# Kernel tuning notes

Hardware: AMD Instinct MI355X
Metric: run time of the kernel (lower is better)

The kernel has to match this reference:

```python
import jax, jax.numpy as jnp
import numpy as np

B, S, IN, OUT = 8, 2048, 4096, 4096
SPARSE_FRACTION = 0.9
ALPHA = 0.3


def setup_inputs() -> dict:
    key = jax.random.key(0)
    k1, k2, k3 = jax.random.split(key, 3)
    total = IN * OUT
    target_nz = int(total * (1.0 - SPARSE_FRACTION))          # nonzeros after rigl step
    num_drop = int(ALPHA * target_nz)                          # = mask.sum() - target_nz
    # kaiming_uniform_(a=sqrt(5)) -> bound = 1/sqrt(fan_in)
    bound = 1.0 / np.sqrt(IN)
    weight = jax.random.uniform(k1, (OUT, IN), minval=-bound, maxval=bound, dtype=jnp.float32)
    x = jax.random.normal(k2, (B, S, IN), dtype=jnp.float32)
    dense_grad = jax.random.normal(k3, (OUT, IN), dtype=jnp.float32) * 0.01
    # mask starts with target_nz + num_drop nonzeros so the drop/grow path runs
    rng = np.random.default_rng(0)
    idx = rng.permutation(total)[: target_nz + num_drop]
    m = np.zeros(total, dtype=bool)
    m[idx] = True
    mask = jnp.asarray(m.reshape(OUT, IN))
    return {"x": x, "weight": weight, "dense_grad": dense_grad, "mask": mask, "num_drop": num_drop}


def _rigl_mask(weight, dense_grad, mask, num_drop):
    # RigL sparse-to-sparse update: drop smallest-|w|, grow largest-|grad| among masked-out slots.
    flat = mask.reshape(-1)
    if num_drop > 0:  # num_drop is a static Python int
        wmag = jnp.abs(weight).reshape(-1)
        _, drop_idx = jax.lax.top_k(-wmag, num_drop)           # smallest magnitudes
        flat = flat.at[drop_idx].set(False)
        gmag = jnp.abs(dense_grad).reshape(-1)
        grow_scores = jnp.where(flat, -jnp.inf, gmag)          # only grow where mask == 0
        _, grow_idx = jax.lax.top_k(grow_scores, num_drop)
        flat = flat.at[grow_idx].set(True)
    return flat.reshape(mask.shape)


def reference(x, weight, dense_grad, mask, num_drop):
    new_mask = _rigl_mask(weight, dense_grad, mask, num_drop)
    masked_weight = weight * new_mask.astype(weight.dtype)     # [OUT, IN]
    # F.linear: y = x @ W^T
    return jnp.einsum('bsi,oi->bso', x, masked_weight)
```

## Files before the change

### kernel.cpp

```cpp
#include <hip/hip_runtime.h>
#include <hip/hip_bf16.h>

#define M_TOT 16384
#define N_TOT 4096
#define K_TOT 4096
#define NELEM 16777216

typedef __attribute__((ext_vector_type(8))) short bf16x8;
typedef __attribute__((ext_vector_type(4))) float f32x4;

#define AS1 __attribute__((address_space(1)))
#define AS3 __attribute__((address_space(3)))

struct SelState {
  unsigned long long prefix;
  unsigned long long thr;
  unsigned int k_rem;
  unsigned int done;
  unsigned int active;
};

struct Ctl {
  unsigned long long pcount;
  unsigned int mask_is_byte;
  unsigned int cand_n;
  SelState d;
  SelState g;
};

__device__ Ctl g_ctl;
__device__ unsigned int g_hist[4096];
__device__ unsigned int g_ticket[4];
__device__ unsigned char g_elig[NELEM];
__device__ unsigned short g_wb[NELEM];
__device__ unsigned short g_xb[(size_t)M_TOT * K_TOT];
__device__ unsigned long long g_cand[NELEM];

__device__ __forceinline__ unsigned short f2bf(float f) {
  unsigned int u = __float_as_uint(f);
  unsigned int r = (u + 0x7FFFu + ((u >> 16) & 1u)) >> 16;
  return (unsigned short)r;
}

__device__ __forceinline__ unsigned long long key_drop_bits(unsigned int fb, int i) {
  unsigned int b = fb & 0x7FFFFFFFu;
  return (((unsigned long long)b) << 24) | (unsigned int)i;
}
__device__ __forceinline__ unsigned long long key_grow_bits(unsigned int fb, int i) {
  unsigned int b = ~(fb & 0x7FFFFFFFu);
  return (((unsigned long long)b) << 24) | (unsigned int)i;
}

__global__ void ctl_reset() {
  int t = threadIdx.x;
  if (t == 0) { g_ctl.pcount = 0ull; g_ctl.cand_n = 0u; }
  if (t < 4) g_ticket[t] = 0u;
  for (int i = t; i < 4096; i += 256) g_hist[i] = 0;
}

__global__ void mask_popcnt(const unsigned int* mw) {
  const int NW = NELEM / 4;
  unsigned int s = 0;
  for (int i = blockIdx.x * blockDim.x + threadIdx.x; i < NW; i += gridDim.x * blockDim.x)
    s += __popc(mw[i]);
  for (int off = 32; off > 0; off >>= 1) s += __shfl_down(s, off, 64);
  if ((threadIdx.x & 63) == 0)
    atomicAdd((unsigned long long*)&g_ctl.pcount, (unsigned long long)s);
}

__global__ void sel_init(const int* ndp) {
  unsigned int k = (unsigned int)ndp[0];
  g_ctl.mask_is_byte = (g_ctl.pcount > 1200000ull) ? 1u : 0u;
  SelState s;
  s.prefix = 0ull; s.thr = 0ull; s.k_rem = k;
  s.done = (k == 0u) ? 1u : 0u;
  s.active = (k > 0u) ? 1u : 0u;
  g_ctl.d = s;
  g_ctl.g = s;
}

__device__ void do_select_impl(unsigned int* hist, SelState* stp, int shift, int nbits) {
  __shared__ unsigned int sc[256];
  __shared__ int tgt;
  const int nb = 1 << nbits;
  const int per = (nb + 255) / 256;
  const int t = threadIdx.x;
  unsigned int s = 0;
  for (int j = 0; j < per; ++j) {
    int b = t * per + j;
    if (b < nb) s += hist[b];
  }
  sc[t] = s;
  __syncthreads();
  for (int off = 1; off < 256; off <<= 1) {
    unsigned int v = (t >= off) ? sc[t - off] : 0u;
    __syncthreads();
    sc[t] += v;
    __syncthreads();
  }
  const unsigned int k = stp->k_rem;
  const unsigned int cum = sc[t];
  const unsigned int before = cum - s;
  if (before < k && k <= cum) tgt = t;
  __syncthreads();
  if (t == tgt) {
    unsigned int c = before;
    for (int j = 0; j < per; ++j) {
      int b = t * per + j;
      unsigned int h = (b < nb) ? hist[b] : 0u;
      if (c + h >= k) {
        unsigned long long np = (stp->prefix << nbits) | (unsigned long long)(unsigned int)b;
        stp->prefix = np;
        stp->k_rem = k - c;
        stp->thr = ((np + 1ull) << shift) - 1ull;
        if (k - c == h) stp->done = 1;
        break;
      }
      c += h;
    }
  }
  __syncthreads();
  for (int b = t; b < nb; b += 256) hist[b] = 0;
}

template <int SEL>
__global__ __launch_bounds__(256) void histsel_full(const float* __restrict__ src) {
  SelState* stp = SEL ? &g_ctl.g : &g_ctl.d;
  if (stp->done) return;
  __shared__ unsigned int lh[4096];
  for (int i = threadIdx.x; i < 4096; i += 256) lh[i] = 0;
  __syncthreads();
  const int N4 = NELEM / 4;
  for (int q = blockIdx.x * blockDim.x + threadIdx.x; q < N4; q += gridDim.x * blockDim.x) {
    float4 v = ((const float4*)src)[q];
    float fv[4] = {v.x, v.y, v.z, v.w};
    unsigned char ev[4] = {1, 1, 1, 1};
    if (SEL) {
      uchar4 e4 = ((const uchar4*)g_elig)[q];
      ev[0] = e4.x; ev[1] = e4.y; ev[2] = e4.z; ev[3] = e4.w;
    }
#pragma unroll
    for (int j = 0; j < 4; ++j) {
      if (SEL && !ev[j]) continue;
      int i = q * 4 + j;
      unsigned int fb = __float_as_uint(fv[j]);
      unsigned long long key = SEL ? key_grow_bits(fb, i) : key_drop_bits(fb, i);
      atomicAdd(&lh[(unsigned int)(key >> 44)], 1u);
    }
  }
  __syncthreads();
  for (int i = threadIdx.x; i < 4096; i += 256)
    if (lh[i]) atomicAdd(&g_hist[i], lh[i]);
  __threadfence();
  __shared__ unsigned int tk;
  if (threadIdx.x == 0) tk = atomicAdd(&g_ticket[SEL], 1u);
  __syncthreads();
  if (tk != (unsigned int)gridDim.x - 1) return;
  __threadfence();
  do_select_impl(g_hist, stp, 44, 12);
}

#define CCAP 4096
template <int SEL>
__global__ __launch_bounds__(256) void compact_pass(const float* __restrict__ src) {
  SelState& st = SEL ? g_ctl.g : g_ctl.d;
  if (st.done) return;
  __shared__ unsigned long long lk[CCAP];
  __shared__ unsigned int ln;
  __shared__ unsigned int gbase;
  if (threadIdx.x == 0) ln = 0;
  __syncthreads();
  const unsigned long long pref = st.prefix;
  const int N4 = NELEM / 4;
  for (int q = blockIdx.x * blockDim.x + threadIdx.x; q < N4; q += gridDim.x * blockDim.x) {
    float4 v = ((const float4*)src)[q];
    float fv[4] = {v.x, v.y, v.z, v.w};
    unsigned char ev[4] = {1, 1, 1, 1};
    if (SEL) {
      uchar4 e4 = ((const uchar4*)g_elig)[q];
      ev[0] = e4.x; ev[1] = e4.y; ev[2] = e4.z; ev[3] = e4.w;
    }
#pragma unroll
    for (int j = 0; j < 4; ++j) {
      if (SEL && !ev[j]) continue;
      int i = q * 4 + j;
      unsigned int fb = __float_as_uint(fv[j]);
      unsigned long long key = SEL ? key_grow_bits(fb, i) : key_drop_bits(fb, i);
      if ((key >> 44) == pref) {
        unsigned int slot = atomicAdd(&ln, 1u);
        if (slot < CCAP) {
          lk[slot] = key;
        } else {
          unsigned int gb = atomicAdd(&g_ctl.cand_n, 1u);
          g_cand[gb] = key;
        }
      }
    }
  }
  __syncthreads();
  unsigned int n = ln < CCAP ? ln : CCAP;
  if (threadIdx.x == 0) gbase = atomicAdd(&g_ctl.cand_n, n);
  __syncthreads();
  for (unsigned int i = threadIdx.x; i < n; i += blockDim.x)
    g_cand[gbase + i] = lk[i];
}

template <int SEL>
__global__ __launch_bounds__(256) void hist_cand(int shift, int nbits) {
  SelState& st = SEL ? g_ctl.g : g_ctl.d;
  if (st.done) return;
  __shared__ unsigned int lh[4096];
  const int nb = 1 << nbits;
  for (int i = threadIdx.x; i < nb; i += blockDim.x) lh[i] = 0;
  __syncthreads();
  const unsigned long long pref = st.prefix;
  const unsigned int n = g_ctl.cand_n;
  for (unsigned int i = blockIdx.x * blockDim.x + threadIdx.x; i < n; i += gridDim.x * blockDim.x) {
    unsigned long long key = g_cand[i];
    if ((key >> (shift + nbits)) == pref)
      atomicAdd(&lh[(unsigned int)(key >> shift) & (unsigned int)(nb - 1)], 1u);
  }
  __syncthreads();
  for (int i = threadIdx.x; i < nb; i += blockDim.x)
    if (lh[i]) atomicAdd(&g_hist[i], lh[i]);
}

template <int SEL>
__global__ void select_pass(int shift, int nbits) {
  SelState* stp = SEL ? &g_ctl.g : &g_ctl.d;
  if (stp->done) return;
  do_select_impl(g_hist, stp, shift, nbits);
}

__global__ __launch_bounds__(256) void build_elig(const float* __restrict__ w, const void* maskp) {
  if (blockIdx.x == 0 && threadIdx.x == 0) g_ctl.cand_n = 0u;
  int q = blockIdx.x * blockDim.x + threadIdx.x;
  if (q >= NELEM / 4) return;
  float4 wv = ((const float4*)w)[q];
  float fv[4] = {wv.x, wv.y, wv.z, wv.w};
  unsigned char m[4];
  if (g_ctl.mask_is_byte) {
    uchar4 m4 = ((const uchar4*)maskp)[q];
    m[0] = m4.x; m[1] = m4.y; m[2] = m4.z; m[3] = m4.w;
  } else {
    int4 m4 = ((const int4*)maskp)[q];
    m[0] = m4.x != 0; m[1] = m4.y != 0; m[2] = m4.z != 0; m[3] = m4.w != 0;
  }
  const bool act = g_ctl.d.active;
  const unsigned long long thr = g_ctl.d.thr;
  uchar4 e;
  unsigned char ev[4];
#pragma unroll
  for (int j = 0; j < 4; ++j) {
    int i = q * 4 + j;
    bool dropped = act && (key_drop_bits(__float_as_uint(fv[j]), i) <= thr);
    ev[j] = (!m[j] || dropped) ? 1 : 0;
  }
  e.x = ev[0]; e.y = ev[1]; e.z = ev[2]; e.w = ev[3];
  ((uchar4*)g_elig)[q] = e;
}

__global__ __launch_bounds__(256) void build_wb(const float* __restrict__ w, const float* __restrict__ gr) {
  int q = blockIdx.x * blockDim.x + threadIdx.x;
  if (q >= NELEM / 4) return;
  float4 wv = ((const float4*)w)[q];
  float4 gv = ((const float4*)gr)[q];
  float wf[4] = {wv.x, wv.y, wv.z, wv.w};
  float gf[4] = {gv.x, gv.y, gv.z, gv.w};
  uchar4 e4 = ((const uchar4*)g_elig)[q];
  unsigned char ev[4] = {e4.x, e4.y, e4.z, e4.w};
  const bool act = g_ctl.g.active;
  const unsigned long long thr = g_ctl.g.thr;
  ushort4 o;
  unsigned short ov[4];
#pragma unroll
  for (int j = 0; j < 4; ++j) {
    int i = q * 4 + j;
    bool keep;
    if (!ev[j]) keep = true;
    else keep = act && (key_grow_bits(__float_as_uint(gf[j]), i) <= thr);
    ov[j] = keep ? f2bf(wf[j]) : (unsigned short)0;
  }
  o.x = ov[0]; o.y = ov[1]; o.z = ov[2]; o.w = ov[3];
  ((ushort4*)g_wb)[q] = o;
}

__global__ __launch_bounds__(256) void convert_x(const float* __restrict__ x) {
  int i = blockIdx.x * blockDim.x + threadIdx.x;
  float4 v = ((const float4*)x)[i];
  ushort4 o;
  o.x = f2bf(v.x); o.y = f2bf(v.y); o.z = f2bf(v.z); o.w = f2bf(v.w);
  ((ushort4*)g_xb)[i] = o;
}

#define BM2 256
#define BN2 256
#define BK2 64
#define NT2 (K_TOT / BK2)
#define BUFB (256 * 128)

__global__ __launch_bounds__(512, 2) void gemm_kernel(float* __restrict__ out) {
  __shared__ __align__(16) char smem[131072];
  unsigned short* Asb = (unsigned short*)smem;
  unsigned short* Bsb = (unsigned short*)(smem + 65536);
  const int tid = threadIdx.x;
  const int lane = tid & 63;
  const int w = tid >> 6;
  const int wm = w >> 2, wn = w & 3;

  const int orig = blockIdx.x;
  const int swz = (orig & 7) * 128 + (orig >> 3);
  const int gm0 = (swz >> 4) * BM2;
  const int gn0 = (swz & 15) * BN2;

  f32x4 acc[8][4];
#pragma unroll
  for (int i = 0; i < 8; ++i)
#pragma unroll
    for (int j = 0; j < 4; ++j) acc[i][j] = (f32x4){0.f, 0.f, 0.f, 0.f};

  const int sr = (w << 3) + (lane >> 3);
  const int sc = 8 * ((lane & 7) ^ (lane >> 3));
  const unsigned short* Agp = g_xb + (size_t)(gm0 + sr) * K_TOT + sc;
  const unsigned short* Bgp = g_wb + (size_t)(gn0 + sr) * K_TOT + sc;
  const int lr = (w << 3);

#define STAGE_A(tile, half) do {                                             \
    const int bi_ = (tile) & 1; const int kb_ = ((tile) & (NT2 - 1)) * BK2;  \
    __builtin_amdgcn_global_load_lds(                                        \
        (const AS1 void*)(Agp + (size_t)((half) * 128) * K_TOT + kb_),       \
        (AS3 void*)(Asb + (size_t)bi_ * (BM2 * BK2) +                        \
                    ((half) * 128 + lr) * BK2), 16, 0, 0);                   \
    __builtin_amdgcn_global_load_lds(                                        \
        (const AS1 void*)(Agp + (size_t)((half) * 128 + 64) * K_TOT + kb_),  \
        (AS3 void*)(Asb + (size_t)bi_ * (BM2 * BK2) +                        \
                    ((half) * 128 + 64 + lr) * BK2), 16, 0, 0);              \
  } while (0)
#define STAGE_B(tile, half) do {                                             \
    const int bi_ = (tile) & 1; const int kb_ = ((tile) & (NT2 - 1)) * BK2;  \
    __builtin_amdgcn_global_load_lds(                                        \
        (const AS1 void*)(Bgp + (size_t)((half) * 128) * K_TOT + kb_),       \
        (AS3 void*)(Bsb + (size_t)bi_ * (BN2 * BK2) +                        \
                    ((half) * 128 + lr) * BK2), 16, 0, 0);                   \
    __builtin_amdgcn_global_load_lds(                                        \
        (const AS1 void*)(Bgp + (size_t)((half) * 128 + 64) * K_TOT + kb_),  \
        (AS3 void*)(Bsb + (size_t)bi_ * (BN2 * BK2) +                        \
                    ((half) * 128 + 64 + lr) * BK2), 16, 0, 0);              \
  } while (0)

  const int r16 = lane & 15;
  const int kcb = (lane >> 4) << 4;
  const int xv = (r16 & 7) << 4;
  const char* Ab0 = (const char*)(Asb + wm * 128 * BK2);
  const char* Bb0 = (const char*)(Bsb + wn * 64 * BK2);

  bf16x8 pA[4][2], pB0[2][2], pB1[2][2];

#define LD_A(qm, bi) do {                                                     \
    const char* ab_ = Ab0 + (bi) * BUFB + ((qm) * 64 + r16) * 128;            \
    _Pragma("unroll") for (int mi = 0; mi < 4; ++mi)                          \
      _Pragma("unroll") for (int sk = 0; sk < 2; ++sk)                        \
        pA[mi][sk] = *(const bf16x8*)(ab_ + mi * 16 * 128 +                   \
                                      ((sk * 64 + kcb) ^ xv));                \
  } while (0)
#define LD_B(P, qn, bi) do {                                                  \
    const char* bb_ = Bb0 + (bi) * BUFB + ((qn) * 32 + r16) * 128;            \
    _Pragma("unroll") for (int nf = 0; nf < 2; ++nf)                          \
      _Pragma("unroll") for (int sk = 0; sk < 2; ++sk)                        \
        P[nf][sk] = *(const bf16x8*)(bb_ + nf * 16 * 128 +                    \
                                     ((sk * 64 + kcb) ^ xv));                 \
  } while (0)
#define MFMA_Q(qm, qn, P) do {                                                \
    __builtin_amdgcn_s_setprio(1);                                            \
    _Pragma("unroll") for (int mi = 0; mi < 4; ++mi)                          \
      _Pragma("unroll") for (int nf = 0; nf < 2; ++nf)                        \
        _Pragma("unroll") for (int sk = 0; sk < 2; ++sk)                      \
          acc[(qm) * 4 + mi][(qn) * 2 + nf] =                                 \
              __builtin_amdgcn_mfma_f32_16x16x32_bf16(                        \
                  pA[mi][sk], P[nf][sk], acc[(qm) * 4 + mi][(qn) * 2 + nf],   \
                  0, 0, 0);                                                   \
    __builtin_amdgcn_s_setprio(0);                                            \
  } while (0)
#define BAR() __builtin_amdgcn_s_barrier()
#define WVM6() asm volatile("s_waitcnt vmcnt(6)" ::: "memory")

  STAGE_A(0, 0); STAGE_A(0, 1); STAGE_B(0, 0); STAGE_B(0, 1);
  STAGE_B(1, 0); STAGE_B(1, 1); STAGE_A(1, 0);
  WVM6();
  BAR();

  for (int it = 0; it < NT2 / 2; ++it) {
    const int T = 2 * it;
    LD_A(0, 0); LD_B(pB0, 0, 0);
    STAGE_A(T + 1, 1);
    BAR();
    MFMA_Q(0, 0, pB0);
    BAR();
    LD_B(pB1, 1, 0);
    STAGE_B(T + 2, 0);
    BAR();
    MFMA_Q(0, 1, pB1);
    BAR();
    LD_A(1, 0);
    STAGE_B(T + 2, 1);
    BAR();
    MFMA_Q(1, 1, pB1);
    BAR();
    STAGE_A(T + 2, 0);
    BAR();
    MFMA_Q(1, 0, pB0);
    WVM6();
    BAR();
    LD_A(0, 1); LD_B(pB0, 0, 1);
    STAGE_A(T + 2, 1);
    BAR();
    MFMA_Q(0, 0, pB0);
    BAR();
    LD_B(pB1, 1, 1);
    STAGE_B(T + 3, 0);
    BAR();
    MFMA_Q(0, 1, pB1);
    BAR();
    LD_A(1, 1);
    STAGE_B(T + 3, 1);
    BAR();
    MFMA_Q(1, 1, pB1);
    BAR();
    STAGE_A(T + 3, 0);
    BAR();
    MFMA_Q(1, 0, pB0);
    WVM6();
    BAR();
  }

  float* lf = (float*)smem;
#pragma unroll
  for (int Q = 0; Q < 4; ++Q) {
    __syncthreads();
#pragma unroll
    for (int m2 = 0; m2 < 2; ++m2) {
      const int rl0 = (wm * 2 + m2) * 16 + (lane >> 4) * 4;
#pragma unroll
      for (int nf = 0; nf < 4; ++nf) {
        const int col = wn * 64 + nf * 16 + (lane & 15);
#pragma unroll
        for (int r = 0; r < 4; ++r)
          lf[(rl0 + r) * 260 + col] = acc[Q * 2 + m2][nf][r];
      }
    }
    __syncthreads();
#pragma unroll
    for (int i2 = 0; i2 < 8; ++i2) {
      const int rl = w * 8 + i2;
      const int grow = (rl >> 5) * 128 + (Q * 2 + ((rl >> 4) & 1)) * 16 + (rl & 15);
      *(float4*)&out[(size_t)(gm0 + grow) * N_TOT + gn0 + lane * 4] =
          *(const float4*)&lf[rl * 260 + lane * 4];
    }
  }
}

extern "C" void kernel_launch(void* const* d_in, const int* in_sizes, int n_in,
                              void* d_out, int out_size, void* d_ws, size_t ws_size,
                              hipStream_t stream) {
  const float* x  = (const float*)d_in[0];
  const float* wt = (const float*)d_in[1];
  const float* gr = (const float*)d_in[2];
  const void*  mk = d_in[3];
  const int*   nd = (const int*)d_in[4];
  (void)d_ws; (void)ws_size; (void)in_sizes; (void)n_in; (void)out_size;

  ctl_reset<<<1, 256, 0, stream>>>();
  mask_popcnt<<<512, 256, 0, stream>>>((const unsigned int*)mk);
  sel_init<<<1, 1, 0, stream>>>(nd);

  const int shifts[5] = {44, 32, 24, 12, 0};
  const int nbits[5]  = {12, 12, 8, 12, 12};

  histsel_full<0><<<1024, 256, 0, stream>>>(wt);
  compact_pass<0><<<1024, 256, 0, stream>>>(wt);
  for (int p = 1; p < 5; ++p) {
    hist_cand<0><<<256, 256, 0, stream>>>(shifts[p], nbits[p]);
    select_pass<0><<<1, 256, 0, stream>>>(shifts[p], nbits[p]);
  }
  build_elig<<<NELEM / 4 / 256, 256, 0, stream>>>(wt, mk);
  histsel_full<1><<<1024, 256, 0, stream>>>(gr);
  compact_pass<1><<<1024, 256, 0, stream>>>(gr);
  for (int p = 1; p < 5; ++p) {
    hist_cand<1><<<256, 256, 0, stream>>>(shifts[p], nbits[p]);
    select_pass<1><<<1, 256, 0, stream>>>(shifts[p], nbits[p]);
  }
  build_wb<<<NELEM / 4 / 256, 256, 0, stream>>>(wt, gr);
  convert_x<<<(M_TOT * K_TOT / 4) / 256, 256, 0, stream>>>(x);
  gemm_kernel<<<1024, 512, 0, stream>>>((float*)d_out);
}
```

Before: 992.1 us.

## Switch GEMM to 32x32x16 MFMA and fuse histogram with select via ticket

The GEMM inner loop now uses 32x32x16 bf16 MFMA tiles with 16-float accumulators in place of 16x16x32 tiles. LDS fragment loads and the epilogue row mapping are reworked to match. The bigger tile is meant to cut LDS read traffic and instruction count per FLOP. Separately, each radix-select pass folds the single-block select into the histogram kernel through a last-block ticket, which removes eight kernel launches. The risks are new ticket-reset and fence correctness issues, plus changed register pressure and a stricter epilogue where only one warp row writes per quarter.

```diff
diff --git a/kernel.cpp b/kernel.cpp
--- a/kernel.cpp
+++ b/kernel.cpp
@@ -8,6 +8,7 @@
 
 typedef __attribute__((ext_vector_type(8))) short bf16x8;
 typedef __attribute__((ext_vector_type(4))) float f32x4;
+typedef __attribute__((ext_vector_type(16))) float f32x16;
 
 #define AS1 __attribute__((address_space(1)))
 #define AS3 __attribute__((address_space(3)))
@@ -206,14 +207,14 @@
 }
 
 template <int SEL>
-__global__ __launch_bounds__(256) void hist_cand(int shift, int nbits) {
-  SelState& st = SEL ? g_ctl.g : g_ctl.d;
-  if (st.done) return;
+__global__ __launch_bounds__(256) void hist_cand_sel(int shift, int nbits) {
+  SelState* stp = SEL ? &g_ctl.g : &g_ctl.d;
+  if (stp->done) return;
   __shared__ unsigned int lh[4096];
   const int nb = 1 << nbits;
   for (int i = threadIdx.x; i < nb; i += blockDim.x) lh[i] = 0;
   __syncthreads();
-  const unsigned long long pref = st.prefix;
+  const unsigned long long pref = stp->prefix;
   const unsigned int n = g_ctl.cand_n;
   for (unsigned int i = blockIdx.x * blockDim.x + threadIdx.x; i < n; i += gridDim.x * blockDim.x) {
     unsigned long long key = g_cand[i];
@@ -223,13 +224,14 @@
   __syncthreads();
   for (int i = threadIdx.x; i < nb; i += blockDim.x)
     if (lh[i]) atomicAdd(&g_hist[i], lh[i]);
-}
-
-template <int SEL>
-__global__ void select_pass(int shift, int nbits) {
-  SelState* stp = SEL ? &g_ctl.g : &g_ctl.d;
-  if (stp->done) return;
+  __threadfence();
+  __shared__ unsigned int tk;
+  if (threadIdx.x == 0) tk = atomicAdd(&g_ticket[2 + SEL], 1u);
+  __syncthreads();
+  if (tk != (unsigned int)gridDim.x - 1) return;
+  __threadfence();
   do_select_impl(g_hist, stp, shift, nbits);
+  if (threadIdx.x == 0) g_ticket[2 + SEL] = 0u;
 }
 
 __global__ __launch_bounds__(256) void build_elig(const float* __restrict__ w, const void* maskp) {
@@ -313,11 +315,13 @@
   const int gm0 = (swz >> 4) * BM2;
   const int gn0 = (swz & 15) * BN2;
 
-  f32x4 acc[8][4];
-#pragma unroll
-  for (int i = 0; i < 8; ++i)
-#pragma unroll
-    for (int j = 0; j < 4; ++j) acc[i][j] = (f32x4){0.f, 0.f, 0.f, 0.f};
+  f32x16 acc[4][2];
+#pragma unroll
+  for (int i = 0; i < 4; ++i)
+#pragma unroll
+    for (int j = 0; j < 2; ++j)
+#pragma unroll
+      for (int r = 0; r < 16; ++r) acc[i][j][r] = 0.f;
 
   const int sr = (w << 3) + (lane >> 3);
   const int sc = 8 * ((lane & 7) ^ (lane >> 3));
@@ -348,37 +352,33 @@
                     ((half) * 128 + 64 + lr) * BK2), 16, 0, 0);              \
   } while (0)
 
-  const int r16 = lane & 15;
-  const int kcb = (lane >> 4) << 4;
-  const int xv = (r16 & 7) << 4;
+  const int r32 = lane & 31;
+  const int hi = lane >> 5;
+  const int xv = (lane & 7) << 4;
   const char* Ab0 = (const char*)(Asb + wm * 128 * BK2);
   const char* Bb0 = (const char*)(Bsb + wn * 64 * BK2);
 
-  bf16x8 pA[4][2], pB0[2][2], pB1[2][2];
+  bf16x8 pA[2][4], pB0[4], pB1[4];
 
 #define LD_A(qm, bi) do {                                                     \
-    const char* ab_ = Ab0 + (bi) * BUFB + ((qm) * 64 + r16) * 128;            \
-    _Pragma("unroll") for (int mi = 0; mi < 4; ++mi)                          \
-      _Pragma("unroll") for (int sk = 0; sk < 2; ++sk)                        \
-        pA[mi][sk] = *(const bf16x8*)(ab_ + mi * 16 * 128 +                   \
-                                      ((sk * 64 + kcb) ^ xv));                \
+    const char* ab_ = Ab0 + (bi) * BUFB + ((qm) * 64 + r32) * 128;            \
+    _Pragma("unroll") for (int mt = 0; mt < 2; ++mt)                          \
+      _Pragma("unroll") for (int ks = 0; ks < 4; ++ks)                        \
+        pA[mt][ks] = *(const bf16x8*)(ab_ + mt * 32 * 128 +                   \
+                                      ((ks * 32 + hi * 16) ^ xv));            \
   } while (0)
 #define LD_B(P, qn, bi) do {                                                  \
-    const char* bb_ = Bb0 + (bi) * BUFB + ((qn) * 32 + r16) * 128;            \
-    _Pragma("unroll") for (int nf = 0; nf < 2; ++nf)                          \
-      _Pragma("unroll") for (int sk = 0; sk < 2; ++sk)                        \
-        P[nf][sk] = *(const bf16x8*)(bb_ + nf * 16 * 128 +                    \
-                                     ((sk * 64 + kcb) ^ xv));                 \
+    const char* bb_ = Bb0 + (bi) * BUFB + ((qn) * 32 + r32) * 128;            \
+    _Pragma("unroll") for (int ks = 0; ks < 4; ++ks)                          \
+      P[ks] = *(const bf16x8*)(bb_ + ((ks * 32 + hi * 16) ^ xv));             \
   } while (0)
 #define MFMA_Q(qm, qn, P) do {                                                \
     __builtin_amdgcn_s_setprio(1);                                            \
-    _Pragma("unroll") for (int mi = 0; mi < 4; ++mi)                          \
-      _Pragma("unroll") for (int nf = 0; nf < 2; ++nf)                        \
-        _Pragma("unroll") for (int sk = 0; sk < 2; ++sk)                      \
-          acc[(qm) * 4 + mi][(qn) * 2 + nf] =                                 \
-              __builtin_amdgcn_mfma_f32_16x16x32_bf16(                        \
-                  pA[mi][sk], P[nf][sk], acc[(qm) * 4 + mi][(qn) * 2 + nf],   \
-                  0, 0, 0);                                                   \
+    _Pragma("unroll") for (int ks = 0; ks < 4; ++ks)                          \
+      _Pragma("unroll") for (int mt = 0; mt < 2; ++mt)                        \
+        acc[(qm) * 2 + mt][qn] =                                              \
+            __builtin_amdgcn_mfma_f32_32x32x16_bf16(                          \
+                pA[mt][ks], P[ks], acc[(qm) * 2 + mt][qn], 0, 0, 0);          \
     __builtin_amdgcn_s_setprio(0);                                            \
   } while (0)
 #define BAR() __builtin_amdgcn_s_barrier()
@@ -437,23 +437,26 @@
 #pragma unroll
   for (int Q = 0; Q < 4; ++Q) {
     __syncthreads();
-#pragma unroll
-    for (int m2 = 0; m2 < 2; ++m2) {
-      const int rl0 = (wm * 2 + m2) * 16 + (lane >> 4) * 4;
-#pragma unroll
-      for (int nf = 0; nf < 4; ++nf) {
-        const int col = wn * 64 + nf * 16 + (lane & 15);
-#pragma unroll
-        for (int r = 0; r < 4; ++r)
-          lf[(rl0 + r) * 260 + col] = acc[Q * 2 + m2][nf][r];
+    if (wm == (Q >> 1)) {
+#pragma unroll
+      for (int mt_rel = 0; mt_rel < 2; ++mt_rel) {
+        const int t = (Q & 1) * 2 + mt_rel;
+#pragma unroll
+        for (int qn = 0; qn < 2; ++qn) {
+          const int col = wn * 64 + qn * 32 + r32;
+#pragma unroll
+          for (int r = 0; r < 16; ++r) {
+            const int rowl = mt_rel * 32 + (r & 3) + 8 * (r >> 2) + 4 * hi;
+            lf[rowl * 260 + col] = acc[t][qn][r];
+          }
+        }
       }
     }
     __syncthreads();
 #pragma unroll
     for (int i2 = 0; i2 < 8; ++i2) {
       const int rl = w * 8 + i2;
-      const int grow = (rl >> 5) * 128 + (Q * 2 + ((rl >> 4) & 1)) * 16 + (rl & 15);
-      *(float4*)&out[(size_t)(gm0 + grow) * N_TOT + gn0 + lane * 4] =
+      *(float4*)&out[(size_t)(gm0 + Q * 64 + rl) * N_TOT + gn0 + lane * 4] =
           *(const float4*)&lf[rl * 260 + lane * 4];
     }
   }
@@ -478,17 +481,13 @@
 
   histsel_full<0><<<1024, 256, 0, stream>>>(wt);
   compact_pass<0><<<1024, 256, 0, stream>>>(wt);
-  for (int p = 1; p < 5; ++p) {
-    hist_cand<0><<<256, 256, 0, stream>>>(shifts[p], nbits[p]);
-    select_pass<0><<<1, 256, 0, stream>>>(shifts[p], nbits[p]);
-  }
+  for (int p = 1; p < 5; ++p)
+    hist_cand_sel<0><<<256, 256, 0, stream>>>(shifts[p], nbits[p]);
   build_elig<<<NELEM / 4 / 256, 256, 0, stream>>>(wt, mk);
   histsel_full<1><<<1024, 256, 0, stream>>>(gr);
   compact_pass<1><<<1024, 256, 0, stream>>>(gr);
-  for (int p = 1; p < 5; ++p) {
-    hist_cand<1><<<256, 256, 0, stream>>>(shifts[p], nbits[p]);
-    select_pass<1><<<1, 256, 0, stream>>>(shifts[p], nbits[p]);
-  }
+  for (int p = 1; p < 5; ++p)
+    hist_cand_sel<1><<<256, 256, 0, stream>>>(shifts[p], nbits[p]);
   build_wb<<<NELEM / 4 / 256, 256, 0, stream>>>(wt, gr);
   convert_x<<<(M_TOT * K_TOT / 4) / 256, 256, 0, stream>>>(x);
   gemm_kernel<<<1024, 512, 0, stream>>>((float*)d_out);
```

Result: no change. 986.5 us (-0.6%).
